# Performance work log

Hardware: AMD Instinct MI355X
Metric: run time of the kernel (lower is better)

## Reference

```python
import jax, jax.numpy as jnp
import numpy as np

D = 64          # hidden_size
NU = 32768      # num user nodes
NI = 16384      # num item nodes
DEG = 50        # mailbox degree (== user_max_length == item_max_length)


def setup_inputs() -> dict:
    key = jax.random.key(0)
    ks = jax.random.split(key, 14)
    s = 1.0 / np.sqrt(D)
    return {
        'user_feat': jax.random.normal(ks[0], (NU, D), jnp.float32),
        'item_feat': jax.random.normal(ks[1], (NI, D), jnp.float32),
        'W_user': jax.random.normal(ks[2], (D, D), jnp.float32) * s,
        'W_item': jax.random.normal(ks[3], (D, D), jnp.float32) * s,
        'gate_u': jax.random.normal(ks[4], (D, 2 * D), jnp.float32) * s,
        'gate_i': jax.random.normal(ks[5], (D, 2 * D), jnp.float32) * s,
        'u_te': jax.random.normal(ks[6], (DEG, D), jnp.float32),
        'u_te_k': jax.random.normal(ks[7], (DEG, D), jnp.float32),
        'i_te': jax.random.normal(ks[8], (DEG, D), jnp.float32),
        'i_te_k': jax.random.normal(ks[9], (DEG, D), jnp.float32),
        'user_nbr': jax.random.randint(ks[10], (NU, DEG), 0, NI, jnp.int32),
        'item_nbr': jax.random.randint(ks[11], (NI, DEG), 0, NU, jnp.int32),
        'user_time': jax.random.randint(ks[12], (NU, DEG), 0, 1000000, jnp.int32),
        'item_time': jax.random.randint(ks[13], (NI, DEG), 0, 1000000, jnp.int32),
    }


def _orgat_att_agg(mail, dst_h, times, te, te_k, gate):
    """One reduce_func: 'orgat' long-term + 'att' short-term, gated concat.
    mail: [N, K, D] neighbor (src) embeddings; dst_h: [N, D]; times: [N, K] int.
    """
    k = times.shape[1]
    # rank of each time within the mailbox, then reversed order index
    order = jnp.argsort(jnp.argsort(times, axis=1), axis=1)
    re_order = k - order - 1                              # [N, K] in [0, K)
    scale = jnp.sqrt(jnp.asarray(mail.shape[-1], mail.dtype))
    # long-term: time-aware attention against dst embedding
    e = jnp.einsum('nkd,nd->nk', te[re_order] + mail, dst_h) / scale
    alpha = jax.nn.softmax(e, axis=1)
    h_long = jnp.einsum('nk,nkd->nd', alpha, mail + te_k[re_order])
    # short-term: attention against most-recent neighbor embedding
    last = jnp.argmax(times, axis=1)                      # [N]
    last_em = jnp.take_along_axis(mail, last[:, None, None], axis=1)[:, 0]
    e1 = jnp.einsum('nkd,nd->nk', mail, last_em) / scale
    alpha1 = jax.nn.softmax(e1, axis=1)
    h_short = jnp.einsum('nk,nkd->nd', alpha1, mail)
    return jnp.concatenate([h_long, h_short], axis=-1) @ gate.T


def reference(user_feat, item_feat, W_user, W_item, gate_u, gate_i,
              u_te, u_te_k, i_te, i_te_k,
              user_nbr, item_nbr, user_time, item_time):
    # linear projections (dropout disabled / eval mode)
    user_h = user_feat @ W_user.T
    item_h = item_feat @ W_item.T
    # item nodes aggregate from neighboring users ('by' relation)
    item_mail = user_h[item_nbr]                          # [NI, DEG, D] gather
    item_new = _orgat_att_agg(item_mail, item_h, item_time, i_te, i_te_k, gate_i)
    # user nodes aggregate from neighboring items ('pby' relation)
    user_mail = item_h[user_nbr]                          # [NU, DEG, D] gather
    user_new = _orgat_att_agg(user_mail, user_h, user_time, u_te, u_te_k, gate_u)
    # residual update with ELU against the pre-projection features
    user_out = jax.nn.elu(user_new + user_feat)
    item_out = jax.nn.elu(item_new + item_feat)
    return user_out, item_out
```

## Files before the change

kernel.cpp:

```cpp
#include <hip/hip_runtime.h>
#include <math.h>

#define NU 32768
#define NI 16384
#define DH 64
#define KK 50

typedef unsigned short ushort_t;
typedef __attribute__((ext_vector_type(8))) short  bf16x8;
typedef __attribute__((ext_vector_type(4))) float  f32x4;
typedef __attribute__((ext_vector_type(4))) unsigned int u32x4;

__device__ __forceinline__ unsigned cvtpk(float lo, float hi) {
    unsigned r;
    asm("v_cvt_pk_bf16_f32 %0, %1, %2" : "=v"(r) : "v"(lo), "v"(hi));
    return r;
}
__device__ __forceinline__ bf16x8 as_bf(u32x4 v) {
    union { u32x4 u; bf16x8 b; } x; x.u = v; return x.b;
}
__device__ __forceinline__ ushort_t bf16r(float v) {
    unsigned u = __float_as_uint(v);
    u += 0x7fffu + ((u >> 16) & 1u);
    return (ushort_t)(u >> 16);
}
__device__ __forceinline__ u32x4 pk8(const float* p) {
    float4 a = *(const float4*)p;
    float4 b = *(const float4*)(p + 4);
    u32x4 r;
    r[0] = cvtpk(a.x, a.y); r[1] = cvtpk(a.z, a.w);
    r[2] = cvtpk(b.x, b.y); r[3] = cvtpk(b.z, b.w);
    return r;
}

__global__ __launch_bounds__(256) void projprep_kernel(
    const float* __restrict__ user_feat, const float* __restrict__ item_feat,
    const float* __restrict__ W_user,    const float* __restrict__ W_item,
    const float* __restrict__ gate_u,    const float* __restrict__ gate_i,
    const float* __restrict__ u_te,      const float* __restrict__ i_te,
    const float* __restrict__ u_te_k,    const float* __restrict__ i_te_k,
    ushort_t* __restrict__ hbf_u, ushort_t* __restrict__ hbf_i,
    ushort_t* __restrict__ teA_u, ushort_t* __restrict__ teA_i,
    ushort_t* __restrict__ gA_u,  ushort_t* __restrict__ gA_i)
{
    __shared__ __align__(16) float SH[3200];
    const int b    = blockIdx.x;
    const int tid  = threadIdx.x;
    const int w    = tid >> 6;
    const int lane = tid & 63;
    const int c = lane & 15, g = lane >> 4;

    if (b < 768) {
        const bool isU = b < 512;
        const float* feat = isU ? user_feat : item_feat;
        const float* W    = isU ? W_user    : W_item;
        ushort_t*    hbf  = isU ? hbf_u     : hbf_i;
        const int    bb   = isU ? b : b - 512;

        ushort_t* WA = (ushort_t*)SH;
        for (int i = tid; i < 4096; i += 256) {
            int j = i & 7, l = (i >> 3) & 63, s = (i >> 9) & 1, mt = i >> 10;
            int row = mt * 16 + (l & 15);
            int k   = s * 32 + ((l >> 4) & 3) * 8 + j;
            WA[i] = bf16r(W[row * DH + k]);
        }
        __syncthreads();

        const int nb = bb * 64 + w * 16;
        u32x4 bf[2];
        #pragma unroll
        for (int s = 0; s < 2; ++s)
            bf[s] = pk8(feat + (size_t)(nb + c) * DH + s * 32 + g * 8);

        #pragma unroll
        for (int mt = 0; mt < 4; ++mt) {
            f32x4 acc = {0.f, 0.f, 0.f, 0.f};
            #pragma unroll
            for (int s = 0; s < 2; ++s) {
                u32x4 af = *(const u32x4*)(WA + ((mt * 2 + s) * 64 + lane) * 8);
                acc = __builtin_amdgcn_mfma_f32_16x16x32_bf16(as_bf(af), as_bf(bf[s]), acc, 0, 0, 0);
            }
            uint2 p;
            p.x = cvtpk(acc[0], acc[1]);
            p.y = cvtpk(acc[2], acc[3]);
            *(uint2*)(hbf + (size_t)(nb + c) * DH + mt * 16 + g * 4) = p;
        }
    } else {
        const int rel = b - 768;
        const float* gate = rel ? gate_i : gate_u;
        const float* te   = rel ? i_te   : u_te;
        const float* tek  = rel ? i_te_k : u_te_k;
        ushort_t* teA = rel ? teA_i : teA_u;
        ushort_t* gA  = rel ? gA_i  : gA_u;
        float* M = SH;

        {
            const int d = w * 16 + c;
            u32x4 ga[2];
            #pragma unroll
            for (int s = 0; s < 2; ++s)
                ga[s] = pk8(gate + (size_t)d * 128 + s * 32 + g * 8);
            #pragma unroll
            for (int rt = 0; rt < 4; ++rt) {
                int r = rt * 16 + c;
                const float* tr = tek + (size_t)(r < KK ? r : 0) * DH;
                f32x4 acc = {0.f, 0.f, 0.f, 0.f};
                #pragma unroll
                for (int s = 0; s < 2; ++s) {
                    u32x4 bfr = pk8(tr + s * 32 + g * 8);
                    acc = __builtin_amdgcn_mfma_f32_16x16x32_bf16(as_bf(ga[s]), as_bf(bfr), acc, 0, 0, 0);
                }
                if (r < KK) {
                    #pragma unroll
                    for (int jj = 0; jj < 4; ++jj)
                        M[(w * 16 + g * 4 + jj) * KK + r] = acc[jj];
                }
            }
        }
        __syncthreads();

        for (int i = tid; i < 4096; i += 256) {
            int j = i & 7, l = (i >> 3) & 63, s = (i >> 9) & 1, t = i >> 10;
            int r = t * 16 + (l & 15);
            int d = s * 32 + ((l >> 4) & 3) * 8 + j;
            teA[i] = bf16r(r < KK ? te[r * DH + d] : 0.f);
        }
        for (int i = tid; i < 12288; i += 256) {
            int j = i & 7, l = (i >> 3) & 63, q = i >> 9;
            int s = q % 6, mt = q / 6;
            int d = mt * 16 + (l & 15);
            int k = s * 32 + ((l >> 4) & 3) * 8 + j;
            float v = 0.f;
            if (k < 128)            v = gate[d * 128 + k];
            else if (k < 128 + KK)  v = M[d * KK + (k - 128)];
            gA[i] = bf16r(v);
        }
    }
}

__global__ __launch_bounds__(256) void agg_kernel(
    const ushort_t* __restrict__ h_src,
    const ushort_t* __restrict__ h_dst,
    const int*      __restrict__ nbr,
    const int*      __restrict__ times,
    const ushort_t* __restrict__ teA,
    ushort_t*       __restrict__ ccout)
{
    __shared__ __align__(16) float EBs[4][192];

    const int wid  = threadIdx.x >> 6;
    const int lane = threadIdx.x & 63;
    const int n    = blockIdx.x * 4 + wid;

    float* EB = EBs[wid];
    const int c = lane & 15;
    const int g = lane >> 4;

    int my_t = 0, my_nb = 0;
    if (lane < KK) {
        my_t  = times[n * KK + lane];
        my_nb = nbr[n * KK + lane];
    }

    u32x4 af[4][2];
    #pragma unroll
    for (int t = 0; t < 4; ++t) {
        int r = t * 16 + c;
        int idx = __builtin_amdgcn_ds_bpermute(r << 2, my_nb);
        const ushort_t* src = h_src + idx * DH;
        #pragma unroll
        for (int s = 0; s < 2; ++s)
            af[t][s] = *(const u32x4*)(src + s * 32 + g * 8);
    }

    int key = my_t * 64 + lane;
    int sro = 0;
    #pragma unroll
    for (int j = 0; j < KK; ++j) {
        int kj = __builtin_amdgcn_readlane(key, j);
        sro += (kj > key) ? 1 : 0;
    }

    int key2 = (lane < KK) ? (my_t * 64 + (63 - lane)) : -1;
    #pragma unroll
    for (int off = 32; off >= 1; off >>= 1) {
        int o = __shfl_xor(key2, off);
        key2 = key2 > o ? key2 : o;
    }
    const int last   = __builtin_amdgcn_readfirstlane(63 - (key2 & 63));
    const int t_last = last >> 4;
    const int c_last = last & 15;

    u32x4 fbv[2];
    {
        const ushort_t* hd = h_dst + n * DH;
        u32x4 sl0, sl1;
        if      (t_last == 0) { sl0 = af[0][0]; sl1 = af[0][1]; }
        else if (t_last == 1) { sl0 = af[1][0]; sl1 = af[1][1]; }
        else if (t_last == 2) { sl0 = af[2][0]; sl1 = af[2][1]; }
        else                  { sl0 = af[3][0]; sl1 = af[3][1]; }
        const int ba = ((lane & 48) + c_last) << 2;
        const bool is1 = (c == 1);
        #pragma unroll
        for (int s = 0; s < 2; ++s) {
            u32x4 dp = *(const u32x4*)(hd + s * 32 + g * 8);
            u32x4 sl = (s == 0) ? sl0 : sl1;
            u32x4 fb;
            #pragma unroll
            for (int u = 0; u < 4; ++u) {
                unsigned sv = (unsigned)__builtin_amdgcn_ds_bpermute(ba, (int)sl[u]);
                fb[u] = is1 ? sv : dp[u];
            }
            fbv[s] = fb;
        }
    }

    #pragma unroll
    for (int t = 0; t < 4; ++t) {
        f32x4 acc = {0.f, 0.f, 0.f, 0.f};
        #pragma unroll
        for (int s = 0; s < 2; ++s)
            acc = __builtin_amdgcn_mfma_f32_16x16x32_bf16(as_bf(af[t][s]), as_bf(fbv[s]), acc, 0, 0, 0);
        if (c < 2) {
            float* eb = EB + c * 64 + t * 16 + g * 4;
            eb[0] = acc[0]; eb[1] = acc[1]; eb[2] = acc[2]; eb[3] = acc[3];
        }
    }

    #pragma unroll
    for (int t = 0; t < 4; ++t) {
        f32x4 acc = {0.f, 0.f, 0.f, 0.f};
        #pragma unroll
        for (int s = 0; s < 2; ++s) {
            u32x4 ta = *(const u32x4*)(teA + ((t * 2 + s) * 64 + lane) * 8);
            acc = __builtin_amdgcn_mfma_f32_16x16x32_bf16(as_bf(ta), as_bf(fbv[s]), acc, 0, 0, 0);
        }
        if (c == 0) {
            float* eb = EB + 128 + t * 16 + g * 4;
            eb[0] = acc[0]; eb[1] = acc[1]; eb[2] = acc[2]; eb[3] = acc[3];
        }
    }

    float eraw  = EB[lane];
    float e1raw = EB[64 + lane];
    float tpown = EB[128 + lane];
    float tps = __uint_as_float(__builtin_amdgcn_ds_bpermute(sro << 2, __float_as_uint(tpown)));
    float e  = (lane < KK) ? (eraw + tps) * 0.125f : -INFINITY;
    float e1 = (lane < KK) ? e1raw * 0.125f        : -INFINITY;
    float m = e, m1 = e1;
    #pragma unroll
    for (int off = 32; off >= 1; off >>= 1) {
        m  = fmaxf(m,  __shfl_xor(m,  off));
        m1 = fmaxf(m1, __shfl_xor(m1, off));
    }
    float p  = (lane < KK) ? __expf(e - m)   : 0.f;
    float p1 = (lane < KK) ? __expf(e1 - m1) : 0.f;
    float s = p, s1 = p1;
    #pragma unroll
    for (int off = 32; off >= 1; off >>= 1) {
        s  += __shfl_xor(s,  off);
        s1 += __shfl_xor(s1, off);
    }
    float al  = p  * __builtin_amdgcn_rcpf(s);
    float al1 = p1 * __builtin_amdgcn_rcpf(s1);

    ushort_t* ccr = ccout + (size_t)n * 192;
    {
        int pushaddr = ((lane < KK) ? sro : lane) << 2;
        float beta = __uint_as_float(__builtin_amdgcn_ds_permute(pushaddr, __float_as_uint(al)));
        ccr[128 + lane] = bf16r(beta);
    }

    unsigned apk = cvtpk(al, al1);
    float hl = 0.f, hs = 0.f;
    #pragma unroll 10
    for (int k = 0; k < KK; ++k) {
        int idx = __builtin_amdgcn_readlane(my_nb, k);
        unsigned a = (unsigned)__builtin_amdgcn_readlane((int)apk, k);
        ushort_t u = h_src[(size_t)idx * DH + lane];
        float mv = __uint_as_float(((unsigned)u) << 16);
        hl = fmaf(__uint_as_float(a << 16), mv, hl);
        hs = fmaf(__uint_as_float(a & 0xffff0000u), mv, hs);
    }
    unsigned hp = cvtpk(hl, hs);
    ccr[lane]      = (ushort_t)hp;
    ccr[64 + lane] = (ushort_t)(hp >> 16);
}

__global__ __launch_bounds__(256) void epi_kernel(
    const ushort_t* __restrict__ cc,
    const ushort_t* __restrict__ gA,
    const float*    __restrict__ feat,
    float*          __restrict__ out)
{
    const int w    = threadIdx.x >> 6;
    const int lane = threadIdx.x & 63;
    const int c = lane & 15, g = lane >> 4;
    const int nb = (blockIdx.x * 4 + w) * 16;

    const char* ccr = (const char*)(cc + (size_t)(nb + c) * 192);
    u32x4 bb6[6];
    #pragma unroll
    for (int s = 0; s < 6; ++s)
        bb6[s] = *(const u32x4*)(ccr + s * 64 + g * 16);

    f32x4 acc[4] = {{0,0,0,0},{0,0,0,0},{0,0,0,0},{0,0,0,0}};
    #pragma unroll
    for (int mt = 0; mt < 4; ++mt)
        #pragma unroll
        for (int s = 0; s < 6; ++s) {
            u32x4 ga = *(const u32x4*)(gA + (size_t)((mt * 6 + s) * 64 + lane) * 8);
            acc[mt] = __builtin_amdgcn_mfma_f32_16x16x32_bf16(as_bf(ga), as_bf(bb6[s]), acc[mt], 0, 0, 0);
        }

    const float* fr   = feat + (size_t)(nb + c) * 64;
    float*       orow = out  + (size_t)(nb + c) * 64;
    #pragma unroll
    for (int mt = 0; mt < 4; ++mt) {
        float4 f4 = *(const float4*)(fr + mt * 16 + g * 4);
        float4 o;
        float v0 = acc[mt][0] + f4.x; o.x = v0 > 0.f ? v0 : (__expf(v0) - 1.f);
        float v1 = acc[mt][1] + f4.y; o.y = v1 > 0.f ? v1 : (__expf(v1) - 1.f);
        float v2 = acc[mt][2] + f4.z; o.z = v2 > 0.f ? v2 : (__expf(v2) - 1.f);
        float v3 = acc[mt][3] + f4.w; o.w = v3 > 0.f ? v3 : (__expf(v3) - 1.f);
        *(float4*)(orow + mt * 16 + g * 4) = o;
    }
}

extern "C" void kernel_launch(void* const* d_in, const int* in_sizes, int n_in,
                              void* d_out, int out_size, void* d_ws, size_t ws_size,
                              hipStream_t stream) {
    const float* user_feat = (const float*)d_in[0];
    const float* item_feat = (const float*)d_in[1];
    const float* W_user    = (const float*)d_in[2];
    const float* W_item    = (const float*)d_in[3];
    const float* gate_u    = (const float*)d_in[4];
    const float* gate_i    = (const float*)d_in[5];
    const float* u_te      = (const float*)d_in[6];
    const float* u_te_k    = (const float*)d_in[7];
    const float* i_te      = (const float*)d_in[8];
    const float* i_te_k    = (const float*)d_in[9];
    const int*   user_nbr  = (const int*)d_in[10];
    const int*   item_nbr  = (const int*)d_in[11];
    const int*   user_time = (const int*)d_in[12];
    const int*   item_time = (const int*)d_in[13];

    ushort_t* hbf_u = (ushort_t*)d_ws;
    ushort_t* hbf_i = hbf_u + NU * DH;
    ushort_t* teA_u = hbf_i + NI * DH;
    ushort_t* teA_i = teA_u + 4096;
    ushort_t* gA_u  = teA_i + 4096;
    ushort_t* gA_i  = gA_u + 12288;
    ushort_t* cc_i  = gA_i + 12288;
    ushort_t* cc_u  = cc_i + (size_t)NI * 192;

    float* user_out = (float*)d_out;
    float* item_out = user_out + NU * DH;

    hipLaunchKernelGGL(projprep_kernel, dim3(770), dim3(256), 0, stream,
                       user_feat, item_feat, W_user, W_item, gate_u, gate_i,
                       u_te, i_te, u_te_k, i_te_k,
                       hbf_u, hbf_i, teA_u, teA_i, gA_u, gA_i);
    hipLaunchKernelGGL(agg_kernel, dim3(NI / 4), dim3(256), 0, stream,
                       hbf_u, hbf_i, item_nbr, item_time, teA_i, cc_i);
    hipLaunchKernelGGL(agg_kernel, dim3(NU / 4), dim3(256), 0, stream,
                       hbf_i, hbf_u, user_nbr, user_time, teA_u, cc_u);
    hipLaunchKernelGGL(epi_kernel, dim3(NI / 64), dim3(256), 0, stream,
                       cc_i, gA_i, item_feat, item_out);
    hipLaunchKernelGGL(epi_kernel, dim3(NU / 64), dim3(256), 0, stream,
                       cc_u, gA_u, user_feat, user_out);
}
```

Baseline: 127.1 us.

## Compute alpha-weighted neighbor aggregation with bf16 MFMA instead of scalar readlane loop

Replaces the per-lane scalar FMA loop over 50 neighbors (readlane of index and alpha, one bf16 load per iteration) with 16x16x32 bf16 MFMA operations. Lanes gather neighbor rows via ds_bpermute, pack alpha weights as the B operand (only two useful columns, long and short), and results are staged through a shared buffer EB before writing. This trades serialized scalar loads and FMAs for batched loads and matrix ops, but wastes most of the MFMA columns and adds LDS round-trips.

```diff
diff --git a/kernel.cpp b/kernel.cpp
--- a/kernel.cpp
+++ b/kernel.cpp
@@ -265,26 +265,59 @@
     float al1 = p1 * __builtin_amdgcn_rcpf(s1);
 
     ushort_t* ccr = ccout + (size_t)n * 192;
+    unsigned apk = cvtpk(al, al1);
     {
         int pushaddr = ((lane < KK) ? sro : lane) << 2;
         float beta = __uint_as_float(__builtin_amdgcn_ds_permute(pushaddr, __float_as_uint(al)));
         ccr[128 + lane] = bf16r(beta);
     }
 
-    unsigned apk = cvtpk(al, al1);
-    float hl = 0.f, hs = 0.f;
-    #pragma unroll 10
-    for (int k = 0; k < KK; ++k) {
-        int idx = __builtin_amdgcn_readlane(my_nb, k);
-        unsigned a = (unsigned)__builtin_amdgcn_readlane((int)apk, k);
-        ushort_t u = h_src[(size_t)idx * DH + lane];
-        float mv = __uint_as_float(((unsigned)u) << 16);
-        hl = fmaf(__uint_as_float(a << 16), mv, hl);
-        hs = fmaf(__uint_as_float(a & 0xffff0000u), mv, hs);
-    }
-    unsigned hp = cvtpk(hl, hs);
-    ccr[lane]      = (ushort_t)hp;
-    ccr[64 + lane] = (ushort_t)(hp >> 16);
+    {
+        f32x4 acc[4] = {{0,0,0,0},{0,0,0,0},{0,0,0,0},{0,0,0,0}};
+        const unsigned sh = (c == 1) ? 16u : 0u;
+        const char* srcb = (const char*)h_src;
+        #pragma unroll
+        for (int s2 = 0; s2 < 2; ++s2) {
+            int va[8];
+            unsigned xb[8];
+            #pragma unroll
+            for (int jv = 0; jv < 8; ++jv) {
+                int r = s2 * 32 + (g << 3) + jv;
+                int idx = __builtin_amdgcn_ds_bpermute(r << 2, my_nb);
+                va[jv] = (idx << 7) + c * 2;
+                unsigned ap = (unsigned)__builtin_amdgcn_ds_bpermute(r << 2, (int)apk);
+                xb[jv] = (ap >> sh) & 0xffffu;
+            }
+            u32x4 bw;
+            #pragma unroll
+            for (int m2 = 0; m2 < 4; ++m2)
+                bw[m2] = xb[2 * m2] | (xb[2 * m2 + 1] << 16);
+            unsigned ld[4][8];
+            #pragma unroll
+            for (int t = 0; t < 4; ++t)
+                #pragma unroll
+                for (int jv = 0; jv < 8; ++jv)
+                    ld[t][jv] = (unsigned)*(const ushort_t*)(srcb + va[jv] + t * 32);
+            #pragma unroll
+            for (int t = 0; t < 4; ++t) {
+                u32x4 aw;
+                #pragma unroll
+                for (int m2 = 0; m2 < 4; ++m2)
+                    aw[m2] = ld[t][2 * m2] | (ld[t][2 * m2 + 1] << 16);
+                acc[t] = __builtin_amdgcn_mfma_f32_16x16x32_bf16(as_bf(aw), as_bf(bw), acc[t], 0, 0, 0);
+            }
+        }
+        if (c < 2) {
+            #pragma unroll
+            for (int t = 0; t < 4; ++t)
+                *(f32x4*)(EB + c * 64 + t * 16 + g * 4) = acc[t];
+        }
+        float hlv = EB[lane];
+        float hsv = EB[64 + lane];
+        unsigned hp = cvtpk(hlv, hsv);
+        ccr[lane]      = (ushort_t)hp;
+        ccr[64 + lane] = (ushort_t)(hp >> 16);
+    }
 }
 
 __global__ __launch_bounds__(256) void epi_kernel(
```

After: 129.8 us. 2.1% more time.
